# Performance work log

Hardware: AMD Instinct MI355X
Metric: run time of the kernel (lower is better)

Reference implementation:

```python
import jax, jax.numpy as jnp
import numpy as np

GRID_SIZE = 5
SPLINE_ORDER = 3


def b_splines(x, grid):
    # x: (B, in), grid: (in, GRID_SIZE + 2*SPLINE_ORDER + 1)
    xe = x[..., None]  # (B, in, 1)
    bases = ((xe >= grid[:, :-1]) & (xe < grid[:, 1:])).astype(x.dtype)
    for k in range(1, SPLINE_ORDER + 1):
        left = (xe - grid[:, : -(k + 1)]) / (grid[:, k:-1] - grid[:, : -(k + 1)])
        right = (grid[:, k + 1:] - xe) / (grid[:, k + 1:] - grid[:, 1:-k])
        bases = left * bases[..., :-1] + right * bases[..., 1:]
    return bases  # (B, in, GRID_SIZE + SPLINE_ORDER)


def kan_linear(x, base_w, spline_w, spline_scaler, grid):
    # efficient-kan KANLinear: base branch + scaled B-spline branch
    base = jax.nn.silu(x) @ base_w.T                       # (B, out)
    b = b_splines(x, grid)                                  # (B, in, G+k)
    scaled = spline_w * spline_scaler[..., None]            # (out, in, G+k)
    spline = jnp.einsum('big,oig->bo', b, scaled)
    return base + spline


def setup_inputs() -> dict:
    key = jax.random.key(0)
    B, T, D, H, O, L = 128, 1024, 512, 512, 256, 2
    GK = GRID_SIZE + SPLINE_ORDER
    stdv = 1.0 / np.sqrt(H)
    ks = jax.random.split(key, 12)
    u = lambda k, shape: jax.random.uniform(k, shape, jnp.float32, -stdv, stdv)
    x = jax.random.normal(ks[0], (B, T, D), jnp.float32)
    wih = u(ks[1], (L, 4 * H, D))
    whh = u(ks[2], (L, 4 * H, H))
    bih = u(ks[3], (L, 4 * H))
    bhh = u(ks[4], (L, 4 * H))
    kan_base = u(ks[5], (L, H, H))
    kan_spline = u(ks[6], (L, H, H, GK))
    kan_scaler = u(ks[7], (L, H, H))
    fc_w = u(ks[8], (O, H))
    fc_b = u(ks[9], (O,))
    # extended B-spline grid, identical per input feature (efficient-kan default)
    h_step = 2.0 / GRID_SIZE
    pts = (np.arange(-SPLINE_ORDER, GRID_SIZE + SPLINE_ORDER + 1) * h_step - 1.0).astype(np.float32)
    grid = jnp.broadcast_to(jnp.asarray(pts), (H, pts.shape[0]))
    return {"x": x, "wih": wih, "whh": whh, "bih": bih, "bhh": bhh,
            "kan_base": kan_base, "kan_spline": kan_spline, "kan_scaler": kan_scaler,
            "grid": grid, "fc_w": fc_w, "fc_b": fc_b}


def reference(x, wih, whh, bih, bhh, kan_base, kan_spline, kan_scaler, grid, fc_w, fc_b):
    L = wih.shape[0]
    B = x.shape[0]
    H = whh.shape[-1]

    def cell(l, inp, h_prev, c_prev):
        gates = inp @ wih[l].T + bih[l] + h_prev @ whh[l].T + bhh[l]
        i, f, g, o = jnp.split(gates, 4, axis=1)
        i = jax.nn.sigmoid(i)
        f = jax.nn.sigmoid(f)
        o = jax.nn.sigmoid(o)
        kan_out = kan_linear(g, kan_base[l], kan_spline[l], kan_scaler[l], grid)
        c_next = f * c_prev + i * kan_out
        h_next = o * jnp.tanh(c_next)
        return h_next, c_next

    def step(carry, x_t):
        h, c = carry  # each (L, B, H)
        inp = x_t
        hs, cs = [], []
        for l in range(L):  # small fixed layer count
            hn, cn = cell(l, inp, h[l], c[l])
            hs.append(hn)
            cs.append(cn)
            inp = hn
        return (jnp.stack(hs), jnp.stack(cs)), None

    h0 = jnp.zeros((L, B, H), x.dtype)
    c0 = jnp.zeros((L, B, H), x.dtype)
    (h_fin, _), _ = jax.lax.scan(step, (h0, c0), jnp.transpose(x, (1, 0, 2)))
    return h_fin[-1] @ fc_w.T + fc_b
```

## Files before the change

### kernel.cpp

```cpp
#include <hip/hip_runtime.h>
#include <hip/hip_fp16.h>


typedef _Float16 f16;
typedef _Float16 half8 __attribute__((ext_vector_type(8)));
typedef float floatx4 __attribute__((ext_vector_type(4)));

#define OFF_H0F   0ULL
#define OFF_H1F   131072ULL
#define OFF_SIG0  262144ULL
#define OFF_SIG1  1048576ULL
#define OFF_A20   1835008ULL
#define OFF_A21   3014656ULL
#define OFF_BAR   4194304ULL
#define WS_NEED   4202496ULL

#define BAR_FLAGS 0
#define BAR_XDONE 512
#define BAR_SEEN  1024

__device__ __forceinline__ half8 cvt8(const float* p) {
  float4 a = *(const float4*)p, b = *(const float4*)(p + 4);
  half8 o;
  o[0]=(f16)a.x; o[1]=(f16)a.y; o[2]=(f16)a.z; o[3]=(f16)a.w;
  o[4]=(f16)b.x; o[5]=(f16)b.y; o[6]=(f16)b.z; o[7]=(f16)b.w;
  return o;
}

__device__ __forceinline__ void st_f16_dc(f16* p, f16 v) {
  union { f16 h; unsigned short u; } cv; cv.h = v;
  unsigned u32 = cv.u;
  asm volatile("global_store_short %0, %1, off sc0 sc1" :: "v"(p), "v"(u32) : "memory");
}
__device__ __forceinline__ void st_f32_dc(float* p, float v) {
  asm volatile("global_store_dword %0, %1, off sc0 sc1" :: "v"(p), "v"(v) : "memory");
}
__device__ __forceinline__ void st_h8_dc(f16* p, half8 v) {
  asm volatile("global_store_dwordx4 %0, %1, off sc0 sc1" :: "v"(p), "v"(v) : "memory");
}

__device__ __forceinline__ void grid_bar(unsigned* bars, int xcc, int iwin,
                                         unsigned rnd, int wgid) {
  asm volatile("s_waitcnt vmcnt(0)" ::: "memory");
  __syncthreads();
  const int tid = threadIdx.x;
  if (tid < 64) {
    if (tid == 0)
      __hip_atomic_store(&bars[BAR_FLAGS + wgid], rnd,
                         __ATOMIC_RELAXED, __HIP_MEMORY_SCOPE_AGENT);
    if (iwin) {
      for (;;) {
        unsigned v0 = __hip_atomic_load(&bars[BAR_FLAGS + tid      ], __ATOMIC_RELAXED, __HIP_MEMORY_SCOPE_AGENT);
        unsigned v1 = __hip_atomic_load(&bars[BAR_FLAGS + tid +  64], __ATOMIC_RELAXED, __HIP_MEMORY_SCOPE_AGENT);
        unsigned v2 = __hip_atomic_load(&bars[BAR_FLAGS + tid + 128], __ATOMIC_RELAXED, __HIP_MEMORY_SCOPE_AGENT);
        unsigned v3 = __hip_atomic_load(&bars[BAR_FLAGS + tid + 192], __ATOMIC_RELAXED, __HIP_MEMORY_SCOPE_AGENT);
        if (__all((v0 >= rnd) && (v1 >= rnd) && (v2 >= rnd) && (v3 >= rnd))) break;
        __builtin_amdgcn_s_sleep(1);
      }
      if (tid == 0) {
        __builtin_amdgcn_fence(__ATOMIC_ACQUIRE, "agent");
        asm volatile("s_waitcnt vmcnt(0)" ::: "memory");
        __hip_atomic_store(&bars[BAR_XDONE + 32*xcc], rnd,
                           __ATOMIC_RELAXED, __HIP_MEMORY_SCOPE_AGENT);
      }
    } else if (tid == 0) {
      while (__hip_atomic_load(&bars[BAR_XDONE + 32*xcc], __ATOMIC_RELAXED, __HIP_MEMORY_SCOPE_AGENT) < rnd)
        __builtin_amdgcn_s_sleep(1);
      asm volatile("s_waitcnt vmcnt(0)\n\tbuffer_inv" ::: "memory");
    }
  }
  __syncthreads();
}

template<int L>
__device__ __forceinline__ void gates_phase(
    int t, int gm, int gn, int mi, int ni, int lane,
    const float* __restrict__ x, const f16* __restrict__ H0, const f16* __restrict__ H1,
    const f16* __restrict__ w1l, float bv,
    float* __restrict__ SIG, f16* __restrict__ A2)
{
  const int arow = gm*32 + mi*16 + (lane & 15);
  const int kq   = (lane >> 4) * 8;
  const half8* bl = (const half8*)w1l + (size_t)ni * 2048;
  floatx4 acc = {0.f, 0.f, 0.f, 0.f};
  if (L == 0) {
    const float* xb = x + (size_t)arow*524288 + (size_t)t*512 + kq;
#pragma unroll
    for (int ks = 0; ks < 16; ++ks) {
      half8 a = cvt8(xb + ks*32);
      acc = __builtin_amdgcn_mfma_f32_16x16x32_f16(a, bl[ks*64 + lane], acc, 0, 0, 0);
    }
    const f16* hb = H0 + (size_t)arow*512 + kq;
#pragma unroll
    for (int ks = 0; ks < 16; ++ks) {
      half8 a = *(const half8*)(hb + ks*32);
      acc = __builtin_amdgcn_mfma_f32_16x16x32_f16(a, bl[(16+ks)*64 + lane], acc, 0, 0, 0);
    }
  } else {
    const f16* hb0 = H0 + (size_t)arow*512 + kq;
#pragma unroll
    for (int ks = 0; ks < 16; ++ks) {
      half8 a = *(const half8*)(hb0 + ks*32);
      acc = __builtin_amdgcn_mfma_f32_16x16x32_f16(a, bl[ks*64 + lane], acc, 0, 0, 0);
    }
    const f16* hb1 = H1 + (size_t)arow*512 + kq;
#pragma unroll
    for (int ks = 0; ks < 16; ++ks) {
      half8 a = *(const half8*)(hb1 + ks*32);
      acc = __builtin_amdgcn_mfma_f32_16x16x32_f16(a, bl[(16+ks)*64 + lane], acc, 0, 0, 0);
    }
  }
  const int cg    = gn*64 + ni*16 + (lane & 15);
  const int chunk = cg >> 9;
  const int mbase = gm*32 + mi*16 + ((lane >> 4) << 2);
#pragma unroll
  for (int r = 0; r < 4; ++r) {
    const int m = mbase + r;
    float v = acc[r] + bv;
    if (chunk == 2) {
      int gcol = cg - 1024;
      float sg = v / (1.f + expf(-v));
      st_f16_dc(A2 + (size_t)m*4608 + gcol, (f16)sg);
      float tp = (v + 2.2f) * 2.5f;
      int c; float u;
      if (tp >= 0.f && tp < 11.f) { c = (int)tp; u = tp - (float)c; }
      else { c = 99; u = 0.f; }
      float u2 = u*u, u3 = u2*u, um = 1.f - u;
      float q0 = um*um*um*(1.f/6.f);
      float q1 = (3.f*u3 - 6.f*u2 + 4.f)*(1.f/6.f);
      float q2 = (-3.f*u3 + 3.f*u2 + 3.f*u + 1.f)*(1.f/6.f);
      float q3 = u3*(1.f/6.f);
      half8 bs;
#pragma unroll
      for (int j = 0; j < 8; ++j) {
        int rr = j - (c - 3);
        float bb = (rr==0)?q0:(rr==1)?q1:(rr==2)?q2:(rr==3)?q3:0.f;
        bs[j] = (f16)bb;
      }
      st_h8_dc(A2 + (size_t)m*4608 + 512 + (size_t)gcol*8, bs);
    } else {
      int scol = (chunk == 3) ? cg - 512 : cg;
      st_f32_dc(SIG + (size_t)m*1536 + scol, 1.f / (1.f + expf(-v)));
    }
  }
}

__device__ __forceinline__ void kan_phase(
    int lane, int wv, int tid, int km, int kn,
    const f16* __restrict__ A2, const half8 (&wb)[36],
    const float* SIG, f16* __restrict__ H,
    float* HFIN, bool writeFin, float& creg, float* __restrict__ red)
{
  const int arow = km*16 + (lane & 15);
  const f16* ab = A2 + (size_t)arow*4608 + wv*576 + ((lane >> 4) << 3);
  floatx4 a0 = {0.f,0.f,0.f,0.f}, a1 = {0.f,0.f,0.f,0.f};
#pragma unroll
  for (int ks = 0; ks < 18; ++ks) {
    half8 a = *(const half8*)(ab + ks*32);
    a0 = __builtin_amdgcn_mfma_f32_16x16x32_f16(a, wb[ks],      a0, 0, 0, 0);
    a1 = __builtin_amdgcn_mfma_f32_16x16x32_f16(a, wb[18 + ks], a1, 0, 0, 0);
  }
  *(floatx4*)&red[((wv*2 + 0)*64 + lane)*4] = a0;
  *(floatx4*)&red[((wv*2 + 1)*64 + lane)*4] = a1;
  __syncthreads();
  const int rm = tid >> 5, cn = tid & 31;
  const int j = cn >> 4;
  const int lsrc = (cn & 15) + ((rm >> 2) << 4);
  const int rr = rm & 3;
  float s = 0.f;
#pragma unroll
  for (int q = 0; q < 8; ++q) s += red[((q*2 + j)*64 + lsrc)*4 + rr];
  const int mg = km*16 + rm, ng = kn*32 + cn;
  float iv = SIG[(size_t)mg*1536 + ng];
  float fv = SIG[(size_t)mg*1536 + 512 + ng];
  float ov = SIG[(size_t)mg*1536 + 1024 + ng];
  float c2 = fv*creg + iv*s;
  float hn = ov * tanhf(c2);
  creg = c2;
  st_f16_dc(H + (size_t)mg*512 + ng, (f16)hn);
  if (writeFin) st_f32_dc(HFIN + (size_t)mg*512 + ng, hn);
}

__launch_bounds__(512, 2)
__global__ void kan_main(const float* __restrict__ x,
                         const float* __restrict__ wih, const float* __restrict__ whh,
                         const float* __restrict__ bih, const float* __restrict__ bhh,
                         const float* __restrict__ kb,  const float* __restrict__ ksp,
                         const float* __restrict__ ksc,
                         const float* __restrict__ fcw, const float* __restrict__ fcb,
                         f16* __restrict__ H0, f16* __restrict__ H1,
                         float* __restrict__ SIG0, float* __restrict__ SIG1,
                         f16* __restrict__ A20, f16* __restrict__ A21,
                         unsigned* __restrict__ bars, float* __restrict__ outp)
{
  extern __shared__ char smem[];
  f16*   w1l = (f16*)smem;
  float* red = (float*)(smem + 131072);
  int*   misc = (int*)(smem + 147456);

  const int tid = threadIdx.x, lane = tid & 63, wv = tid >> 6;
  const int w = blockIdx.x, lw = w >> 7, wl = w & 127;
  const int gm = wl & 3, gn = wl >> 2;
  const int mi = wv & 1, ni = wv >> 1;
  const int km = wl & 7, kn = wl >> 3;

  int xcc;
  asm("s_getreg_b32 %0, hwreg(HW_REG_XCC_ID)" : "=s"(xcc));

  if (tid == 0) {
    unsigned old = __hip_atomic_fetch_add(&bars[BAR_SEEN + 32*xcc], 1u,
                       __ATOMIC_RELAXED, __HIP_MEMORY_SCOPE_AGENT);
    misc[0] = (old == 0);
  }

  for (int u = tid; u < 8192; u += 512) {
    int lu = u & 63, t2 = u >> 6;
    int ks = t2 & 31, n2 = t2 >> 5;
    int n = gn*64 + n2*16 + (lu & 15);
    int k = ks*32 + ((lu >> 4) << 3);
    const float* src = (k < 512) ? (wih + ((size_t)lw*2048 + n)*512 + k)
                                 : (whh + ((size_t)lw*2048 + n)*512 + (k - 512));
    ((half8*)w1l)[u] = cvt8(src);
  }
  half8 wb[36];
#pragma unroll
  for (int jt = 0; jt < 2; ++jt)
#pragma unroll
  for (int ks = 0; ks < 18; ++ks) {
    int n = kn*32 + jt*16 + (lane & 15);
    int k = wv*576 + ks*32 + ((lane >> 4) << 3);
    half8 o;
    if (k < 512) {
      o = cvt8(kb + ((size_t)lw*512 + n)*512 + k);
    } else {
      int i = (k - 512) >> 3;
      float sc = ksc[((size_t)lw*512 + n)*512 + i];
      const float* sp = ksp + (((size_t)lw*512 + n)*512 + i)*8;
      float4 a = *(const float4*)sp, b2 = *(const float4*)(sp + 4);
      o[0]=(f16)(a.x*sc);  o[1]=(f16)(a.y*sc);  o[2]=(f16)(a.z*sc);  o[3]=(f16)(a.w*sc);
      o[4]=(f16)(b2.x*sc); o[5]=(f16)(b2.y*sc); o[6]=(f16)(b2.z*sc); o[7]=(f16)(b2.w*sc);
    }
    wb[jt*18 + ks] = o;
  }
  const int cg = gn*64 + ni*16 + (lane & 15);
  const float bv = bih[lw*2048 + cg] + bhh[lw*2048 + cg];

  float creg = 0.f;
  float* SIGl = lw ? SIG1 : SIG0;
  f16*   A2l  = lw ? A21  : A20;
  f16*   Hl   = lw ? H1   : H0;
  float* HFIN = SIG0;

  __syncthreads();
  const int iwin = misc[0];
  unsigned rnd = 0;

  for (int tau = 0; tau <= 1024; ++tau) {
    const bool act = lw ? (tau >= 1) : (tau < 1024);
    const int  t   = lw ? tau - 1 : tau;
    if (act) {
      if (lw == 0) gates_phase<0>(t, gm, gn, mi, ni, lane, x, H0, H1, w1l, bv, SIGl, A2l);
      else         gates_phase<1>(t, gm, gn, mi, ni, lane, x, H0, H1, w1l, bv, SIGl, A2l);
    }
    ++rnd; grid_bar(bars, xcc, iwin, rnd, w);
    if (act)
      kan_phase(lane, wv, tid, km, kn, A2l, wb, SIGl, Hl, HFIN,
                (lw == 1) && (t == 1023), creg, red);
    ++rnd; grid_bar(bars, xcc, iwin, rnd, w);
  }

  if (w < 64) {
    int idx = w*512 + tid, m = idx >> 8, o = idx & 255;
    const float4* hr = (const float4*)(HFIN + (size_t)m*512);
    const float4* wr = (const float4*)(fcw  + (size_t)o*512);
    float s = fcb[o];
#pragma unroll 4
    for (int q = 0; q < 128; ++q) {
      float4 a = hr[q], b = wr[q];
      s += a.x*b.x + a.y*b.y + a.z*b.z + a.w*b.w;
    }
    outp[idx] = s;
  }
}

extern "C" void kernel_launch(void* const* d_in, const int* in_sizes, int n_in,
                              void* d_out, int out_size, void* d_ws, size_t ws_size,
                              hipStream_t stream) {
  (void)in_sizes; (void)n_in;
  if (ws_size < WS_NEED) {
    hipMemsetAsync(d_out, 0, (size_t)out_size * 4, stream);
    return;
  }
  const float* x   = (const float*)d_in[0];
  const float* wih = (const float*)d_in[1];
  const float* whh = (const float*)d_in[2];
  const float* bih = (const float*)d_in[3];
  const float* bhh = (const float*)d_in[4];
  const float* kb  = (const float*)d_in[5];
  const float* ksp = (const float*)d_in[6];
  const float* ksc = (const float*)d_in[7];
  const float* fcw = (const float*)d_in[9];
  const float* fcb = (const float*)d_in[10];

  char* ws = (char*)d_ws;
  f16*   H0   = (f16*)(ws + OFF_H0F);
  f16*   H1   = (f16*)(ws + OFF_H1F);
  float* SIG0 = (float*)(ws + OFF_SIG0);
  float* SIG1 = (float*)(ws + OFF_SIG1);
  f16*   A20  = (f16*)(ws + OFF_A20);
  f16*   A21  = (f16*)(ws + OFF_A21);
  unsigned* bars = (unsigned*)(ws + OFF_BAR);

  hipMemsetAsync(ws + OFF_H0F, 0, 262144, stream);
  hipMemsetAsync(ws + OFF_BAR, 0, 8192, stream);

  hipFuncSetAttribute((const void*)kan_main, hipFuncAttributeMaxDynamicSharedMemorySize, 147712);
  kan_main<<<dim3(256), dim3(512), 147712, stream>>>(
      x, wih, whh, bih, bhh, kb, ksp, ksc, fcw, fcb,
      H0, H1, SIG0, SIG1, A20, A21, bars, (float*)d_out);
}
```

Before: 27.89 ms.

## Partition work by batch slab per XCD and replace grid barrier with slab barriers

Work is re-partitioned so that each 16-row batch slab is handled entirely by the 32 workgroups on one XCD, covering both layers and all gate columns. The global grid-wide barrier is then replaced by per-slab barriers. When the XCD placement is verified as 32 workgroups per XCD, stores use XCD-local cache scope (sc0 only) and skip agent fences. This aims to cut cross-die synchronisation and coherence traffic on every one of the roughly 2050 barriers. The recurrent weights now sit in registers while the input weights stay in LDS, and the final FC layer reads its rows through LDS. A fallback path with a generic mapping is kept in case placement differs, at the cost of an extra initial grid barrier and higher register pressure.

```diff
diff --git a/kernel.cpp b/kernel.cpp
--- a/kernel.cpp
+++ b/kernel.cpp
@@ -6,18 +6,23 @@
 typedef _Float16 half8 __attribute__((ext_vector_type(8)));
 typedef float floatx4 __attribute__((ext_vector_type(4)));
 
-#define OFF_H0F   0ULL
-#define OFF_H1F   131072ULL
+#define OFF_H0    0ULL
+#define OFF_H1    131072ULL
 #define OFF_SIG0  262144ULL
 #define OFF_SIG1  1048576ULL
 #define OFF_A20   1835008ULL
 #define OFF_A21   3014656ULL
-#define OFF_BAR   4194304ULL
-#define WS_NEED   4202496ULL
-
-#define BAR_FLAGS 0
-#define BAR_XDONE 512
-#define BAR_SEEN  1024
+#define OFF_HFIN  4194304ULL
+#define OFF_BAR   4456448ULL
+#define WS_NEED   4476928ULL
+
+#define IDX_FLAGS 0
+#define IDX_XD    1024
+#define IDX_SEEN  2048
+#define IDX_GFLAG 3072
+#define IDX_GDONE 4096
+
+#define MFMA(acc, a, b) acc = __builtin_amdgcn_mfma_f32_16x16x32_f16(a, b, acc, 0, 0, 0)
 
 __device__ __forceinline__ half8 cvt8(const float* p) {
   float4 a = *(const float4*)p, b = *(const float4*)(p + 4);
@@ -27,100 +32,125 @@
   return o;
 }
 
-__device__ __forceinline__ void st_f16_dc(f16* p, f16 v) {
-  union { f16 h; unsigned short u; } cv; cv.h = v;
-  unsigned u32 = cv.u;
-  asm volatile("global_store_short %0, %1, off sc0 sc1" :: "v"(p), "v"(u32) : "memory");
-}
-__device__ __forceinline__ void st_f32_dc(float* p, float v) {
-  asm volatile("global_store_dword %0, %1, off sc0 sc1" :: "v"(p), "v"(v) : "memory");
-}
-__device__ __forceinline__ void st_h8_dc(f16* p, half8 v) {
-  asm volatile("global_store_dwordx4 %0, %1, off sc0 sc1" :: "v"(p), "v"(v) : "memory");
-}
-
-__device__ __forceinline__ void grid_bar(unsigned* bars, int xcc, int iwin,
-                                         unsigned rnd, int wgid) {
+template<bool LOC> __device__ __forceinline__ void st_f16(f16* p, f16 v) {
+  union { f16 h; unsigned short u; } c; c.h = v; unsigned u32 = c.u;
+  if (LOC) asm volatile("global_store_short %0, %1, off sc0"     :: "v"(p), "v"(u32) : "memory");
+  else     asm volatile("global_store_short %0, %1, off sc0 sc1" :: "v"(p), "v"(u32) : "memory");
+}
+template<bool LOC> __device__ __forceinline__ void st_f32(float* p, float v) {
+  if (LOC) asm volatile("global_store_dword %0, %1, off sc0"     :: "v"(p), "v"(v) : "memory");
+  else     asm volatile("global_store_dword %0, %1, off sc0 sc1" :: "v"(p), "v"(v) : "memory");
+}
+template<bool LOC> __device__ __forceinline__ void st_h8(f16* p, half8 v) {
+  if (LOC) asm volatile("global_store_dwordx4 %0, %1, off sc0"     :: "v"(p), "v"(v) : "memory");
+  else     asm volatile("global_store_dwordx4 %0, %1, off sc0 sc1" :: "v"(p), "v"(v) : "memory");
+}
+
+template<bool LOC>
+__device__ __forceinline__ void slab_bar(unsigned* bars, int slab, int role, unsigned rnd) {
   asm volatile("s_waitcnt vmcnt(0)" ::: "memory");
+  __syncthreads();
+  const int tid = threadIdx.x;
+  if (!LOC) {
+    if (tid == 0) __builtin_amdgcn_fence(__ATOMIC_RELEASE, "agent");
+  }
+  if (tid < 64) {
+    if (tid == 0)
+      __hip_atomic_store(&bars[IDX_FLAGS + slab*32 + role], rnd,
+                         __ATOMIC_RELAXED, __HIP_MEMORY_SCOPE_AGENT);
+    if (role == 0) {
+      unsigned* fl = &bars[IDX_FLAGS + slab*32 + (tid & 31)];
+      for (;;) {
+        unsigned v = __hip_atomic_load(fl, __ATOMIC_RELAXED, __HIP_MEMORY_SCOPE_AGENT);
+        if (__all((tid >= 32) || (v >= rnd))) break;
+        __builtin_amdgcn_s_sleep(1);
+      }
+      if (tid == 0) {
+        if (!LOC) __builtin_amdgcn_fence(__ATOMIC_ACQUIRE, "agent");
+        __hip_atomic_store(&bars[IDX_XD + slab*32], rnd,
+                           __ATOMIC_RELAXED, __HIP_MEMORY_SCOPE_AGENT);
+      }
+    } else if (tid == 0) {
+      while (__hip_atomic_load(&bars[IDX_XD + slab*32],
+                 __ATOMIC_RELAXED, __HIP_MEMORY_SCOPE_AGENT) < rnd)
+        __builtin_amdgcn_s_sleep(1);
+      if (!LOC) __builtin_amdgcn_fence(__ATOMIC_ACQUIRE, "agent");
+    }
+  }
+  __syncthreads();
+  asm volatile("buffer_inv" ::: "memory");
+}
+
+__device__ __forceinline__ void init_gbar(unsigned* bars, int w) {
   __syncthreads();
   const int tid = threadIdx.x;
   if (tid < 64) {
     if (tid == 0)
-      __hip_atomic_store(&bars[BAR_FLAGS + wgid], rnd,
-                         __ATOMIC_RELAXED, __HIP_MEMORY_SCOPE_AGENT);
-    if (iwin) {
+      __hip_atomic_store(&bars[IDX_GFLAG + w], 1u, __ATOMIC_RELAXED, __HIP_MEMORY_SCOPE_AGENT);
+    if (w == 0) {
       for (;;) {
-        unsigned v0 = __hip_atomic_load(&bars[BAR_FLAGS + tid      ], __ATOMIC_RELAXED, __HIP_MEMORY_SCOPE_AGENT);
-        unsigned v1 = __hip_atomic_load(&bars[BAR_FLAGS + tid +  64], __ATOMIC_RELAXED, __HIP_MEMORY_SCOPE_AGENT);
-        unsigned v2 = __hip_atomic_load(&bars[BAR_FLAGS + tid + 128], __ATOMIC_RELAXED, __HIP_MEMORY_SCOPE_AGENT);
-        unsigned v3 = __hip_atomic_load(&bars[BAR_FLAGS + tid + 192], __ATOMIC_RELAXED, __HIP_MEMORY_SCOPE_AGENT);
-        if (__all((v0 >= rnd) && (v1 >= rnd) && (v2 >= rnd) && (v3 >= rnd))) break;
+        unsigned v0 = __hip_atomic_load(&bars[IDX_GFLAG + tid      ], __ATOMIC_RELAXED, __HIP_MEMORY_SCOPE_AGENT);
+        unsigned v1 = __hip_atomic_load(&bars[IDX_GFLAG + tid +  64], __ATOMIC_RELAXED, __HIP_MEMORY_SCOPE_AGENT);
+        unsigned v2 = __hip_atomic_load(&bars[IDX_GFLAG + tid + 128], __ATOMIC_RELAXED, __HIP_MEMORY_SCOPE_AGENT);
+        unsigned v3 = __hip_atomic_load(&bars[IDX_GFLAG + tid + 192], __ATOMIC_RELAXED, __HIP_MEMORY_SCOPE_AGENT);
+        if (__all(v0 && v1 && v2 && v3)) break;
         __builtin_amdgcn_s_sleep(1);
       }
-      if (tid == 0) {
-        __builtin_amdgcn_fence(__ATOMIC_ACQUIRE, "agent");
-        asm volatile("s_waitcnt vmcnt(0)" ::: "memory");
-        __hip_atomic_store(&bars[BAR_XDONE + 32*xcc], rnd,
-                           __ATOMIC_RELAXED, __HIP_MEMORY_SCOPE_AGENT);
-      }
+      if (tid == 0)
+        __hip_atomic_store(&bars[IDX_GDONE], 1u, __ATOMIC_RELAXED, __HIP_MEMORY_SCOPE_AGENT);
     } else if (tid == 0) {
-      while (__hip_atomic_load(&bars[BAR_XDONE + 32*xcc], __ATOMIC_RELAXED, __HIP_MEMORY_SCOPE_AGENT) < rnd)
+      while (!__hip_atomic_load(&bars[IDX_GDONE], __ATOMIC_RELAXED, __HIP_MEMORY_SCOPE_AGENT))
         __builtin_amdgcn_s_sleep(1);
-      asm volatile("s_waitcnt vmcnt(0)\n\tbuffer_inv" ::: "memory");
-    }
-  }
-  __syncthreads();
-}
-
-template<int L>
+    }
+  }
+  __syncthreads();
+}
+
+template<int L, bool LOC>
 __device__ __forceinline__ void gates_phase(
-    int t, int gm, int gn, int mi, int ni, int lane,
+    int t, int slab, int sub, int wv, int lane,
     const float* __restrict__ x, const f16* __restrict__ H0, const f16* __restrict__ H1,
-    const f16* __restrict__ w1l, float bv,
+    const f16* wlds, const half8 (&wgr)[16], float bv,
     float* __restrict__ SIG, f16* __restrict__ A2)
 {
-  const int arow = gm*32 + mi*16 + (lane & 15);
-  const int kq   = (lane >> 4) * 8;
-  const half8* bl = (const half8*)w1l + (size_t)ni * 2048;
+  const int m  = slab*16 + (lane & 15);
+  const int kq = (lane >> 4) * 8;
+  const half8* bl = (const half8*)wlds + (size_t)wv * 1024;
   floatx4 acc = {0.f, 0.f, 0.f, 0.f};
+
   if (L == 0) {
-    const float* xb = x + (size_t)arow*524288 + (size_t)t*512 + kq;
+    const float* xb = x + (size_t)m*524288 + (size_t)t*512 + kq;
 #pragma unroll
     for (int ks = 0; ks < 16; ++ks) {
       half8 a = cvt8(xb + ks*32);
-      acc = __builtin_amdgcn_mfma_f32_16x16x32_f16(a, bl[ks*64 + lane], acc, 0, 0, 0);
-    }
-    const f16* hb = H0 + (size_t)arow*512 + kq;
+      MFMA(acc, a, bl[ks*64 + lane]);
+    }
+  } else {
+    const f16* hb0 = H0 + (size_t)m*512 + kq;
+#pragma unroll
+    for (int ks = 0; ks < 16; ++ks) {
+      half8 a = *(const half8*)(hb0 + ks*32);
+      MFMA(acc, a, bl[ks*64 + lane]);
+    }
+  }
+  {
+    const f16* hb = ((L == 0) ? H0 : H1) + (size_t)m*512 + kq;
 #pragma unroll
     for (int ks = 0; ks < 16; ++ks) {
       half8 a = *(const half8*)(hb + ks*32);
-      acc = __builtin_amdgcn_mfma_f32_16x16x32_f16(a, bl[(16+ks)*64 + lane], acc, 0, 0, 0);
-    }
-  } else {
-    const f16* hb0 = H0 + (size_t)arow*512 + kq;
-#pragma unroll
-    for (int ks = 0; ks < 16; ++ks) {
-      half8 a = *(const half8*)(hb0 + ks*32);
-      acc = __builtin_amdgcn_mfma_f32_16x16x32_f16(a, bl[ks*64 + lane], acc, 0, 0, 0);
-    }
-    const f16* hb1 = H1 + (size_t)arow*512 + kq;
-#pragma unroll
-    for (int ks = 0; ks < 16; ++ks) {
-      half8 a = *(const half8*)(hb1 + ks*32);
-      acc = __builtin_amdgcn_mfma_f32_16x16x32_f16(a, bl[(16+ks)*64 + lane], acc, 0, 0, 0);
-    }
-  }
-  const int cg    = gn*64 + ni*16 + (lane & 15);
+      MFMA(acc, a, wgr[ks]);
+    }
+  }
+  const int cg    = sub*128 + wv*16 + (lane & 15);
   const int chunk = cg >> 9;
-  const int mbase = gm*32 + mi*16 + ((lane >> 4) << 2);
+  const int rbase = slab*16 + ((lane >> 4) << 2);
 #pragma unroll
   for (int r = 0; r < 4; ++r) {
-    const int m = mbase + r;
+    const int m2 = rbase + r;
     float v = acc[r] + bv;
     if (chunk == 2) {
-      int gcol = cg - 1024;
-      float sg = v / (1.f + expf(-v));
-      st_f16_dc(A2 + (size_t)m*4608 + gcol, (f16)sg);
+      const int gcol = cg - 1024;
+      st_f16<LOC>(A2 + (size_t)m2*4608 + gcol, (f16)(v / (1.f + expf(-v))));
       float tp = (v + 2.2f) * 2.5f;
       int c; float u;
       if (tp >= 0.f && tp < 11.f) { c = (int)tp; u = tp - (float)c; }
@@ -137,28 +167,29 @@
         float bb = (rr==0)?q0:(rr==1)?q1:(rr==2)?q2:(rr==3)?q3:0.f;
         bs[j] = (f16)bb;
       }
-      st_h8_dc(A2 + (size_t)m*4608 + 512 + (size_t)gcol*8, bs);
+      st_h8<LOC>(A2 + (size_t)m2*4608 + 512 + (size_t)gcol*8, bs);
     } else {
-      int scol = (chunk == 3) ? cg - 512 : cg;
-      st_f32_dc(SIG + (size_t)m*1536 + scol, 1.f / (1.f + expf(-v)));
-    }
-  }
-}
-
+      const int scol = (chunk == 3) ? (cg - 512) : cg;
+      st_f32<LOC>(SIG + (size_t)m2*1536 + scol, 1.f / (1.f + expf(-v)));
+    }
+  }
+}
+
+template<bool LOC>
 __device__ __forceinline__ void kan_phase(
-    int lane, int wv, int tid, int km, int kn,
+    bool writeFin, int slab, int sub, int wv, int lane, int tid,
     const f16* __restrict__ A2, const half8 (&wb)[36],
-    const float* SIG, f16* __restrict__ H,
-    float* HFIN, bool writeFin, float& creg, float* __restrict__ red)
+    const float* __restrict__ SIG, f16* __restrict__ H,
+    float* __restrict__ HFIN, float& creg, float* __restrict__ red)
 {
-  const int arow = km*16 + (lane & 15);
-  const f16* ab = A2 + (size_t)arow*4608 + wv*576 + ((lane >> 4) << 3);
+  const int m = slab*16 + (lane & 15);
+  const f16* ab = A2 + (size_t)m*4608 + wv*576 + ((lane >> 4) << 3);
   floatx4 a0 = {0.f,0.f,0.f,0.f}, a1 = {0.f,0.f,0.f,0.f};
 #pragma unroll
   for (int ks = 0; ks < 18; ++ks) {
     half8 a = *(const half8*)(ab + ks*32);
-    a0 = __builtin_amdgcn_mfma_f32_16x16x32_f16(a, wb[ks],      a0, 0, 0, 0);
-    a1 = __builtin_amdgcn_mfma_f32_16x16x32_f16(a, wb[18 + ks], a1, 0, 0, 0);
+    MFMA(a0, a, wb[ks*2]);
+    MFMA(a1, a, wb[ks*2 + 1]);
   }
   *(floatx4*)&red[((wv*2 + 0)*64 + lane)*4] = a0;
   *(floatx4*)&red[((wv*2 + 1)*64 + lane)*4] = a1;
@@ -170,64 +201,52 @@
   float s = 0.f;
 #pragma unroll
   for (int q = 0; q < 8; ++q) s += red[((q*2 + j)*64 + lsrc)*4 + rr];
-  const int mg = km*16 + rm, ng = kn*32 + cn;
+  const int mg = slab*16 + rm, ng = sub*32 + cn;
   float iv = SIG[(size_t)mg*1536 + ng];
   float fv = SIG[(size_t)mg*1536 + 512 + ng];
   float ov = SIG[(size_t)mg*1536 + 1024 + ng];
   float c2 = fv*creg + iv*s;
   float hn = ov * tanhf(c2);
   creg = c2;
-  st_f16_dc(H + (size_t)mg*512 + ng, (f16)hn);
-  if (writeFin) st_f32_dc(HFIN + (size_t)mg*512 + ng, hn);
-}
-
-__launch_bounds__(512, 2)
-__global__ void kan_main(const float* __restrict__ x,
-                         const float* __restrict__ wih, const float* __restrict__ whh,
-                         const float* __restrict__ bih, const float* __restrict__ bhh,
-                         const float* __restrict__ kb,  const float* __restrict__ ksp,
-                         const float* __restrict__ ksc,
-                         const float* __restrict__ fcw, const float* __restrict__ fcb,
-                         f16* __restrict__ H0, f16* __restrict__ H1,
-                         float* __restrict__ SIG0, float* __restrict__ SIG1,
-                         f16* __restrict__ A20, f16* __restrict__ A21,
-                         unsigned* __restrict__ bars, float* __restrict__ outp)
+  st_f16<LOC>(H + (size_t)mg*512 + ng, (f16)hn);
+  if (writeFin) st_f32<LOC>(HFIN + (size_t)mg*512 + ng, hn);
+}
+
+template<bool LOC>
+__device__ void run_all(int slab, int role, int tid, int lane, int wv,
+    const float* __restrict__ x, const float* __restrict__ wih, const float* __restrict__ whh,
+    const float* __restrict__ bih, const float* __restrict__ bhh,
+    const float* __restrict__ kb, const float* __restrict__ ksp, const float* __restrict__ ksc,
+    const float* __restrict__ fcw, const float* __restrict__ fcb,
+    f16* H0, f16* H1, float* SIG0, float* SIG1, f16* A20, f16* A21, float* HFIN,
+    unsigned* bars, float* outp, char* smem)
 {
-  extern __shared__ char smem[];
-  f16*   w1l = (f16*)smem;
-  float* red = (float*)(smem + 131072);
-  int*   misc = (int*)(smem + 147456);
-
-  const int tid = threadIdx.x, lane = tid & 63, wv = tid >> 6;
-  const int w = blockIdx.x, lw = w >> 7, wl = w & 127;
-  const int gm = wl & 3, gn = wl >> 2;
-  const int mi = wv & 1, ni = wv >> 1;
-  const int km = wl & 7, kn = wl >> 3;
-
-  int xcc;
-  asm("s_getreg_b32 %0, hwreg(HW_REG_XCC_ID)" : "=s"(xcc));
-
-  if (tid == 0) {
-    unsigned old = __hip_atomic_fetch_add(&bars[BAR_SEEN + 32*xcc], 1u,
-                       __ATOMIC_RELAXED, __HIP_MEMORY_SCOPE_AGENT);
-    misc[0] = (old == 0);
-  }
+  f16*   wlds = (f16*)smem;
+  float* red  = (float*)(smem + 131072);
+  const int lw = role >> 4, sub = role & 15;
 
   for (int u = tid; u < 8192; u += 512) {
     int lu = u & 63, t2 = u >> 6;
-    int ks = t2 & 31, n2 = t2 >> 5;
-    int n = gn*64 + n2*16 + (lu & 15);
+    int ks = t2 & 15, nt = t2 >> 4;
+    int n = sub*128 + nt*16 + (lu & 15);
     int k = ks*32 + ((lu >> 4) << 3);
-    const float* src = (k < 512) ? (wih + ((size_t)lw*2048 + n)*512 + k)
-                                 : (whh + ((size_t)lw*2048 + n)*512 + (k - 512));
-    ((half8*)w1l)[u] = cvt8(src);
+    ((half8*)wlds)[u] = cvt8(wih + ((size_t)lw*2048 + n)*512 + k);
+  }
+  half8 wgr[16];
+  {
+    int n = sub*128 + wv*16 + (lane & 15);
+#pragma unroll
+    for (int ks = 0; ks < 16; ++ks) {
+      int k = ks*32 + ((lane >> 4) << 3);
+      wgr[ks] = cvt8(whh + ((size_t)lw*2048 + n)*512 + k);
+    }
   }
   half8 wb[36];
 #pragma unroll
   for (int jt = 0; jt < 2; ++jt)
 #pragma unroll
   for (int ks = 0; ks < 18; ++ks) {
-    int n = kn*32 + jt*16 + (lane & 15);
+    int n = sub*32 + jt*16 + (lane & 15);
     int k = wv*576 + ks*32 + ((lane >> 4) << 3);
     half8 o;
     if (k < 512) {
@@ -240,46 +259,97 @@
       o[0]=(f16)(a.x*sc);  o[1]=(f16)(a.y*sc);  o[2]=(f16)(a.z*sc);  o[3]=(f16)(a.w*sc);
       o[4]=(f16)(b2.x*sc); o[5]=(f16)(b2.y*sc); o[6]=(f16)(b2.z*sc); o[7]=(f16)(b2.w*sc);
     }
-    wb[jt*18 + ks] = o;
-  }
-  const int cg = gn*64 + ni*16 + (lane & 15);
+    wb[ks*2 + jt] = o;
+  }
+  const int cg = sub*128 + wv*16 + (lane & 15);
   const float bv = bih[lw*2048 + cg] + bhh[lw*2048 + cg];
 
-  float creg = 0.f;
   float* SIGl = lw ? SIG1 : SIG0;
   f16*   A2l  = lw ? A21  : A20;
   f16*   Hl   = lw ? H1   : H0;
-  float* HFIN = SIG0;
-
-  __syncthreads();
-  const int iwin = misc[0];
+  float creg = 0.f;
+
+  __syncthreads();
   unsigned rnd = 0;
 
   for (int tau = 0; tau <= 1024; ++tau) {
     const bool act = lw ? (tau >= 1) : (tau < 1024);
-    const int  t   = lw ? tau - 1 : tau;
+    const int  t   = lw ? (tau - 1) : tau;
     if (act) {
-      if (lw == 0) gates_phase<0>(t, gm, gn, mi, ni, lane, x, H0, H1, w1l, bv, SIGl, A2l);
-      else         gates_phase<1>(t, gm, gn, mi, ni, lane, x, H0, H1, w1l, bv, SIGl, A2l);
-    }
-    ++rnd; grid_bar(bars, xcc, iwin, rnd, w);
+      if (lw == 0) gates_phase<0, LOC>(t, slab, sub, wv, lane, x, H0, H1, wlds, wgr, bv, SIGl, A2l);
+      else         gates_phase<1, LOC>(t, slab, sub, wv, lane, x, H0, H1, wlds, wgr, bv, SIGl, A2l);
+    }
+    ++rnd; slab_bar<LOC>(bars, slab, role, rnd);
     if (act)
-      kan_phase(lane, wv, tid, km, kn, A2l, wb, SIGl, Hl, HFIN,
-                (lw == 1) && (t == 1023), creg, red);
-    ++rnd; grid_bar(bars, xcc, iwin, rnd, w);
-  }
-
-  if (w < 64) {
-    int idx = w*512 + tid, m = idx >> 8, o = idx & 255;
-    const float4* hr = (const float4*)(HFIN + (size_t)m*512);
-    const float4* wr = (const float4*)(fcw  + (size_t)o*512);
+      kan_phase<LOC>((lw == 1) && (t == 1023), slab, sub, wv, lane, tid,
+                     A2l, wb, SIGl, Hl, HFIN, creg, red);
+    ++rnd; slab_bar<LOC>(bars, slab, role, rnd);
+  }
+
+  if (role < 8) {
+    const int rrow = tid >> 8;
+    const int col  = tid & 255;
+    const float* src = HFIN + (size_t)(slab*16 + role*2 + rrow)*512;
+    red[rrow*512 + col]       = src[col];
+    red[rrow*512 + 256 + col] = src[256 + col];
+    __syncthreads();
+    const int o = tid & 255, r2 = tid >> 8;
+    const float* wr = fcw + (size_t)o*512;
+    const float* hr = red + r2*512;
     float s = fcb[o];
 #pragma unroll 4
     for (int q = 0; q < 128; ++q) {
-      float4 a = hr[q], b = wr[q];
-      s += a.x*b.x + a.y*b.y + a.z*b.z + a.w*b.w;
-    }
-    outp[idx] = s;
+      float4 b = *(const float4*)(wr + q*4);
+      s += hr[q*4]*b.x + hr[q*4+1]*b.y + hr[q*4+2]*b.z + hr[q*4+3]*b.w;
+    }
+    outp[(size_t)(slab*16 + role*2 + r2)*256 + o] = s;
+  }
+}
+
+__launch_bounds__(512, 2)
+__global__ void kan_main(const float* __restrict__ x,
+                         const float* __restrict__ wih, const float* __restrict__ whh,
+                         const float* __restrict__ bih, const float* __restrict__ bhh,
+                         const float* __restrict__ kb,  const float* __restrict__ ksp,
+                         const float* __restrict__ ksc,
+                         const float* __restrict__ fcw, const float* __restrict__ fcb,
+                         f16* H0, f16* H1, float* SIG0, float* SIG1,
+                         f16* A20, f16* A21, float* HFIN,
+                         unsigned* bars, float* outp)
+{
+  extern __shared__ char smem[];
+  volatile int* misc = (volatile int*)(smem + 147456);
+  const int tid = threadIdx.x, lane = tid & 63, wv = tid >> 6, w = blockIdx.x;
+
+  int xcc;
+  asm("s_getreg_b32 %0, hwreg(HW_REG_XCC_ID)" : "=s"(xcc));
+  xcc &= 7;
+
+  if (tid == 0) {
+    unsigned old = __hip_atomic_fetch_add(&bars[IDX_SEEN + xcc*32], 1u,
+                       __ATOMIC_RELAXED, __HIP_MEMORY_SCOPE_AGENT);
+    misc[0] = (int)old;
+  }
+  init_gbar(bars, w);
+  if (tid == 0) {
+    int ok = 1;
+    for (int e = 0; e < 8; ++e)
+      ok &= (__hip_atomic_load(&bars[IDX_SEEN + e*32],
+                __ATOMIC_RELAXED, __HIP_MEMORY_SCOPE_AGENT) == 32u);
+    misc[1] = ok;
+  }
+  __syncthreads();
+  const int rank = misc[0];
+  const int locm = misc[1];
+
+  if (locm) {
+    int slab = __builtin_amdgcn_readfirstlane(xcc);
+    int role = __builtin_amdgcn_readfirstlane(rank);
+    run_all<true >(slab, role, tid, lane, wv, x, wih, whh, bih, bhh, kb, ksp, ksc,
+                   fcw, fcb, H0, H1, SIG0, SIG1, A20, A21, HFIN, bars, outp, smem);
+  } else {
+    run_all<false>(w >> 5, w & 31, tid, lane, wv, x, wih, whh, bih, bhh, kb, ksp, ksc,
+                   fcw, fcb, H0, H1, SIG0, SIG1, A20, A21, HFIN, bars, outp, smem);
   }
 }
 
@@ -303,19 +373,20 @@
   const float* fcb = (const float*)d_in[10];
 
   char* ws = (char*)d_ws;
-  f16*   H0   = (f16*)(ws + OFF_H0F);
-  f16*   H1   = (f16*)(ws + OFF_H1F);
+  f16*   H0   = (f16*)(ws + OFF_H0);
+  f16*   H1   = (f16*)(ws + OFF_H1);
   float* SIG0 = (float*)(ws + OFF_SIG0);
   float* SIG1 = (float*)(ws + OFF_SIG1);
   f16*   A20  = (f16*)(ws + OFF_A20);
   f16*   A21  = (f16*)(ws + OFF_A21);
+  float* HFIN = (float*)(ws + OFF_HFIN);
   unsigned* bars = (unsigned*)(ws + OFF_BAR);
 
-  hipMemsetAsync(ws + OFF_H0F, 0, 262144, stream);
-  hipMemsetAsync(ws + OFF_BAR, 0, 8192, stream);
+  hipMemsetAsync(ws + OFF_H0, 0, 262144, stream);
+  hipMemsetAsync(ws + OFF_BAR, 0, 20480, stream);
 
   hipFuncSetAttribute((const void*)kan_main, hipFuncAttributeMaxDynamicSharedMemorySize, 147712);
   kan_main<<<dim3(256), dim3(512), 147712, stream>>>(
       x, wih, whh, bih, bhh, kb, ksp, ksc, fcw, fcb,
-      H0, H1, SIG0, SIG1, A20, A21, bars, (float*)d_out);
-}
+      H0, H1, SIG0, SIG1, A20, A21, HFIN, bars, (float*)d_out);
+}
```

Result: faster. 25.71 ms (-7.8%).
